# Kernel optimization log

Hardware: AMD Instinct MI355X
Metric: run time of the kernel (lower is better)

## Reference

```python
import jax, jax.numpy as jnp
import numpy as np

H = 48  # hidden_size


def _lstm_cell(inp, h, c, Wih, Whh, bih, bhh):
    # PyTorch LSTMCell: gates ordered (i, f, g, o)
    gates = inp @ Wih.T + h @ Whh.T + bih + bhh
    i, f, g, o = jnp.split(gates, 4, axis=-1)
    i = jax.nn.sigmoid(i)
    f = jax.nn.sigmoid(f)
    g = jnp.tanh(g)
    o = jax.nn.sigmoid(o)
    c_new = f * c + i * g
    h_new = o * jnp.tanh(c_new)
    return h_new, c_new


def setup_inputs() -> dict:
    key = jax.random.key(0)
    ks = jax.random.split(key, 8)
    B, T = 4096, 512
    s = 0.1
    return {
        "x": jax.random.normal(ks[0], (B, T), dtype=jnp.float32),
        "W_ih0": jax.random.normal(ks[1], (4 * H, 1), dtype=jnp.float32) * s,
        "W_hh0": jax.random.normal(ks[2], (4 * H, H), dtype=jnp.float32) * s,
        "b_ih0": jnp.full((4 * H,), 0.01, dtype=jnp.float32),
        "b_hh0": jnp.full((4 * H,), 0.01, dtype=jnp.float32),
        "W_ih1": jax.random.normal(ks[3], (4 * H, H), dtype=jnp.float32) * s,
        "W_hh1": jax.random.normal(ks[4], (4 * H, H), dtype=jnp.float32) * s,
        "b_ih1": jnp.full((4 * H,), 0.01, dtype=jnp.float32),
        "b_hh1": jnp.full((4 * H,), 0.01, dtype=jnp.float32),
        "W_lin": jax.random.normal(ks[5], (1, H), dtype=jnp.float32) * s,
        "b_lin": jnp.full((1,), 0.01, dtype=jnp.float32),
        "future_pred": 64,
    }


def reference(x, W_ih0, W_hh0, b_ih0, b_hh0, W_ih1, W_hh1, b_ih1, b_hh1,
              W_lin, b_lin, future_pred):
    B = x.shape[0]
    h0 = jnp.zeros((B, H), dtype=jnp.float32)
    c0 = jnp.zeros((B, H), dtype=jnp.float32)
    h1 = jnp.zeros((B, H), dtype=jnp.float32)
    c1 = jnp.zeros((B, H), dtype=jnp.float32)

    def tick(h0, c0, h1, c1, inp):  # inp: [B,1]
        h0, c0 = _lstm_cell(inp, h0, c0, W_ih0, W_hh0, b_ih0, b_hh0)
        h1, c1 = _lstm_cell(h0, h1, c1, W_ih1, W_hh1, b_ih1, b_hh1)
        out = h1 @ W_lin.T + b_lin  # [B,1]
        return h0, c0, h1, c1, out

    # teacher-forced pass over observed sequence
    def step_obs(carry, xt):
        h0, c0, h1, c1 = carry
        h0, c0, h1, c1, out = tick(h0, c0, h1, c1, xt)
        return (h0, c0, h1, c1), out

    xs = jnp.swapaxes(x, 0, 1)[:, :, None]  # [T, B, 1]
    (h0, c0, h1, c1), outs_obs = jax.lax.scan(step_obs, (h0, c0, h1, c1), xs)
    last_out = outs_obs[-1]

    def step_fut(carry, _):
        h0, c0, h1, c1, out = carry
        h0, c0, h1, c1, out = tick(h0, c0, h1, c1, out)
        return (h0, c0, h1, c1, out), out

    _, outs_fut = jax.lax.scan(step_fut, (h0, c0, h1, c1, last_out), None,
                               length=future_pred)

    outs = jnp.concatenate([outs_obs, outs_fut], axis=0)  # [T+F, B, 1]
    return jnp.swapaxes(outs[:, :, 0], 0, 1)  # [B, T+F]
```

## Files before the change

kernel.cpp:

```cpp
#include <hip/hip_runtime.h>

#define T_OBS 512
#define RSTRH 264
#define PSTR  28
#define L2E   1.44269504089f

typedef float    f32x4 __attribute__((ext_vector_type(4)));
typedef _Float16 f16x8 __attribute__((ext_vector_type(8)));

#define MF(A,B,C) __builtin_amdgcn_mfma_f32_16x16x32_f16(A,B,C,0,0,0)

__device__ __forceinline__ unsigned f2h(float f){
    union { _Float16 h; unsigned short u; } v; v.h=(_Float16)f; return (unsigned)v.u;
}

__device__ __forceinline__ void bar_lds(){
    asm volatile("s_waitcnt lgkmcnt(0)" ::: "memory");
    __builtin_amdgcn_sched_barrier(0);
    __builtin_amdgcn_s_barrier();
    __builtin_amdgcn_sched_barrier(0);
}

__device__ __forceinline__ float act1(const f32x4 a, float& c){
    const float Ei=__builtin_amdgcn_exp2f(a[0]), Ef=__builtin_amdgcn_exp2f(a[1]);
    const float Eg=__builtin_amdgcn_exp2f(a[2]), Eo=__builtin_amdgcn_exp2f(a[3]);
    const float ui=1.f+Ei, uf=1.f+Ef, ug=1.f+Eg, uo=1.f+Eo;
    const float P=ui*uf, Q=ug*uo;
    const float R=__builtin_amdgcn_rcpf(P*Q);
    const float aP=R*Q, aQ=R*P;
    const float ig=aP*uf, fg=aP*ui;
    const float og=aQ*ug;
    const float gg=fmaf(aQ*uo,-2.f,1.f);
    c = fg*c + ig*gg;
    const float Ec=__builtin_amdgcn_exp2f(2.f*L2E*c);
    return og*fmaf(__builtin_amdgcn_rcpf(1.f+Ec),-2.f,1.f);
}

__device__ __forceinline__ int u_of_pos(const int p){
    return 8*(p>>3) + 4*(p&1) + ((p&7)>>1);
}

__global__ __launch_bounds__(768, 1) void lstm2_v10(
    const float* __restrict__ x,
    const float* __restrict__ Wih0, const float* __restrict__ Whh0,
    const float* __restrict__ bih0, const float* __restrict__ bhh0,
    const float* __restrict__ Wih1, const float* __restrict__ Whh1,
    const float* __restrict__ bih1, const float* __restrict__ bhh1,
    const float* __restrict__ Wlin, const float* __restrict__ blin,
    const int* __restrict__ fut,
    float* __restrict__ out)
{
    __shared__ __attribute__((aligned(16))) _Float16 s_h[16 * RSTRH];
    __shared__ __attribute__((aligned(16))) float s_pr[2][16 * PSTR];
    unsigned* const s32 = (unsigned*)s_h;

    const int tid  = threadIdx.x;
    const int wave = tid >> 6, lane = tid & 63;
    const int q    = lane & 15, rg = lane >> 4;
    const bool isL1 = (wave >= 6);
    const int  w    = isL1 ? wave - 6 : wave;

    for (int i = tid; i < 16 * RSTRH; i += 768) s_h[i] = (_Float16)0.f;

    const float sgl = ((q & 3) == 2) ? 2.f * L2E : -L2E;

    f16x8 ah[2][3], al[2][3];
    #pragma unroll
    for (int i = 0; i < 2; ++i) {
        const int t  = 2 * w + i;
        const int rp = 16 * t + q;
        const int r0 = (rp & 3) * 48 + (rp >> 2);
        #pragma unroll
        for (int s = 0; s < 3; ++s)
            #pragma unroll
            for (int j = 0; j < 8; ++j) {
                const int p = 32 * s + 8 * rg + j;
                float v = 0.f;
                if (isL1) v = ((p < 48) ? Wih1[r0 * 48 + u_of_pos(p)]
                                        : Whh1[r0 * 48 + u_of_pos(p - 48)]) * sgl;
                else if (p < 48) v = Whh0[r0 * 48 + u_of_pos(p)] * sgl;
                const _Float16 hi = (_Float16)v;
                ah[i][s][j] = hi;
                al[i][s][j] = (_Float16)(v - (float)hi);
            }
    }

    const float sg4[4] = { -L2E, -L2E, 2.f * L2E, -L2E };
    f32x4 bvt[2], wi0v[2];
    float wlq[2];
    #pragma unroll
    for (int i = 0; i < 2; ++i) {
        const int u = 8 * w + 4 * i + rg;
        wlq[i] = Wlin[u];
        #pragma unroll
        for (int g = 0; g < 4; ++g) {
            bvt[i][g]  = (isL1 ? (bih1[g*48+u] + bhh1[g*48+u])
                               : (bih0[g*48+u] + bhh0[g*48+u])) * sg4[g];
            wi0v[i][g] = Wih0[g * 48 + u] * sg4[g];
        }
    }

    int koff[3];
    #pragma unroll
    for (int s = 0; s < 3; ++s) {
        const int p0 = 32 * s + 8 * rg;
        koff[s] = p0 + ((p0 >= 48) ? 80 : 0);
    }

    const int F    = fut[0];
    const int TT   = T_OBS + F;
    const int bb0  = blockIdx.x * 16;
    const float bl = blin[0];
    const int xrow = (bb0 + q) * T_OBS;
    const int nbh  = q * RSTRH;
    const int hwp  = nbh + (isL1 ? 128 : 0) + 8 * w + 2 * rg;
    const int prw  = q * PSTR + 4 * w + rg;

    float cc0 = 0.f, cc1 = 0.f;
    const f32x4 z4 = { 0.f, 0.f, 0.f, 0.f };

    __syncthreads();

    if (!isL1) {
        const float x0 = x[xrow];
        const f32x4 a0 = bvt[0] + wi0v[0] * x0;
        const f32x4 a1 = bvt[1] + wi0v[1] * x0;
        const unsigned h0 = f2h(act1(a0, cc0));
        const unsigned h1 = f2h(act1(a1, cc1));
        s32[hwp >> 1] = h0 | (h1 << 16);
    }
    bar_lds();
    float xcur = isL1 ? 0.f : x[xrow + 1];

#define STEADY(TAU_, CB_, PB_) do {                                              \
    if (!isL1) {                                                                 \
        const float xnxt = x[xrow + (((TAU_) + 1 < T_OBS) ? (TAU_) + 1 : T_OBS - 1)]; \
        if ((TAU_) >= 2 && wave == 0) {           \
            const int nn = lane >> 2, j0 = lane & 3;                             \
            const float* pr = &s_pr[((TAU_) - 1) & 1][nn * PSTR];                \
            float sg = pr[j0] + pr[j0+4] + pr[j0+8] + pr[j0+12]                  \
                     + pr[j0+16] + pr[j0+20];                                    \
            sg += __shfl_xor(sg, 1); sg += __shfl_xor(sg, 2);                    \
            if (j0 == 0) out[(bb0 + nn) * TT + ((TAU_) - 2)] = sg + bl;          \
        }                                                                        \
        const f16x8 B0 = *(const f16x8*)(s_h + nbh + (PB_) + koff[0]);           \
        const f16x8 B1 = *(const f16x8*)(s_h + nbh + (PB_) + koff[1]);           \
        f32x4 Aq[2], Bq[2];                                                      \
        _Pragma("unroll")                                                        \
        for (int i = 0; i < 2; ++i) {                                            \
            Aq[i] = MF(ah[i][0], B0, bvt[i]);                                    \
            Aq[i] = MF(al[i][0], B0, Aq[i]);                                     \
            Bq[i] = MF(ah[i][1], B1, z4);                                        \
            Bq[i] = MF(al[i][1], B1, Bq[i]);                                     \
        }                                                                        \
        const f32x4 a0 = Aq[0] + Bq[0] + wi0v[0] * xcur;                         \
        const f32x4 a1 = Aq[1] + Bq[1] + wi0v[1] * xcur;                         \
        const unsigned h0 = f2h(act1(a0, cc0));                                  \
        const unsigned h1 = f2h(act1(a1, cc1));                                  \
        s32[(hwp + (CB_)) >> 1] = h0 | (h1 << 16);                               \
        xcur = xnxt;                                                             \
    } else {                                                                     \
        const f16x8 B0 = *(const f16x8*)(s_h + nbh + (PB_) + koff[0]);           \
        const f16x8 B1 = *(const f16x8*)(s_h + nbh + (PB_) + koff[1]);           \
        const f16x8 B2 = *(const f16x8*)(s_h + nbh + (PB_) + koff[2]);           \
        f32x4 Aq[2], Bq[2];                                                      \
        _Pragma("unroll")                                                        \
        for (int i = 0; i < 2; ++i) {                                            \
            Aq[i] = MF(ah[i][0], B0, bvt[i]);                                    \
            Aq[i] = MF(al[i][0], B0, Aq[i]);                                     \
            Aq[i] = MF(ah[i][1], B1, Aq[i]);                                     \
            Bq[i] = MF(al[i][1], B1, z4);                                        \
            Bq[i] = MF(ah[i][2], B2, Bq[i]);                                     \
            Bq[i] = MF(al[i][2], B2, Bq[i]);                                     \
        }                                                                        \
        const f32x4 a0 = Aq[0] + Bq[0];                                          \
        const f32x4 a1 = Aq[1] + Bq[1];                                          \
        const float h0 = act1(a0, cc0);                                          \
        const float h1 = act1(a1, cc1);                                          \
        s32[(hwp + (CB_)) >> 1] = f2h(h0) | (f2h(h1) << 16);                     \
        s_pr[(TAU_) & 1][prw] = fmaf(h1, wlq[1], h0 * wlq[0]);                   \
    }                                                                            \
    bar_lds();                                                                   \
} while (0)

    for (int tau = 1; tau < T_OBS - 1; tau += 2) {
        STEADY(tau,     64, 0);
        STEADY(tau + 1,  0, 64);
    }
    STEADY(T_OBS - 1, 64, 0);

    if (tid < 16) {
        const float* pr = &s_pr[1][tid * PSTR];
        const f32x4 sv = *(const f32x4*)(pr)      + *(const f32x4*)(pr + 4)
                       + *(const f32x4*)(pr + 8)  + *(const f32x4*)(pr + 12)
                       + *(const f32x4*)(pr + 16) + *(const f32x4*)(pr + 20);
        out[(bb0 + tid) * TT + (T_OBS - 2)] = sv[0] + sv[1] + sv[2] + sv[3] + bl;
    }

    for (int tau = T_OBS; tau <= TT; ++tau) {
        const int cb = (tau & 1) * 64;
        const int pb = cb ^ 64;

        f32x4 Aq[2], Bq[2];
        if (isL1) {
            const f16x8 B0 = *(const f16x8*)(s_h + nbh + pb + koff[0]);
            const f16x8 B1 = *(const f16x8*)(s_h + nbh + pb + koff[1]);
            const f16x8 B2 = *(const f16x8*)(s_h + nbh + pb + koff[2]);
            #pragma unroll
            for (int i = 0; i < 2; ++i) {
                Aq[i] = MF(ah[i][0], B0, bvt[i]);
                Aq[i] = MF(al[i][0], B0, Aq[i]);
                Aq[i] = MF(ah[i][1], B1, Aq[i]);
                Bq[i] = MF(al[i][1], B1, z4);
                Bq[i] = MF(ah[i][2], B2, Bq[i]);
                Bq[i] = MF(al[i][2], B2, Bq[i]);
            }
            const f32x4 a0 = Aq[0] + Bq[0];
            const f32x4 a1 = Aq[1] + Bq[1];
            const float h0 = act1(a0, cc0);
            const float h1 = act1(a1, cc1);
            s32[(hwp + cb) >> 1] = f2h(h0) | (f2h(h1) << 16);
            s_pr[tau & 1][prw] = fmaf(h1, wlq[1], h0 * wlq[0]);
        } else {
            const f16x8 B0 = *(const f16x8*)(s_h + nbh + pb + koff[0]);
            const f16x8 B1 = *(const f16x8*)(s_h + nbh + pb + koff[1]);
            #pragma unroll
            for (int i = 0; i < 2; ++i) {
                Aq[i] = MF(ah[i][0], B0, bvt[i]);
                Aq[i] = MF(al[i][0], B0, Aq[i]);
                Bq[i] = MF(ah[i][1], B1, z4);
                Bq[i] = MF(al[i][1], B1, Bq[i]);
            }
        }
        bar_lds();

        if (!isL1) {
            const float* pr = &s_pr[tau & 1][q * PSTR];
            const f32x4 sv = *(const f32x4*)(pr)      + *(const f32x4*)(pr + 4)
                           + *(const f32x4*)(pr + 8)  + *(const f32x4*)(pr + 12)
                           + *(const f32x4*)(pr + 16) + *(const f32x4*)(pr + 20);
            const float o = sv[0] + sv[1] + sv[2] + sv[3] + bl;
            if (tid < 16) out[(bb0 + q) * TT + (tau - 1)] = o;
            if (tau < TT) {
                const f32x4 a0 = Aq[0] + Bq[0] + wi0v[0] * o;
                const f32x4 a1 = Aq[1] + Bq[1] + wi0v[1] * o;
                const unsigned h0 = f2h(act1(a0, cc0));
                const unsigned h1 = f2h(act1(a1, cc1));
                s32[(hwp + cb) >> 1] = h0 | (h1 << 16);
            }
        }
        bar_lds();
    }
}

extern "C" void kernel_launch(void* const* d_in, const int* in_sizes, int n_in,
                              void* d_out, int out_size, void* d_ws, size_t ws_size,
                              hipStream_t stream) {
    const float* x    = (const float*)d_in[0];
    const float* Wih0 = (const float*)d_in[1];
    const float* Whh0 = (const float*)d_in[2];
    const float* bih0 = (const float*)d_in[3];
    const float* bhh0 = (const float*)d_in[4];
    const float* Wih1 = (const float*)d_in[5];
    const float* Whh1 = (const float*)d_in[6];
    const float* bih1 = (const float*)d_in[7];
    const float* bhh1 = (const float*)d_in[8];
    const float* Wlin = (const float*)d_in[9];
    const float* blin = (const float*)d_in[10];
    const int*   fut  = (const int*)d_in[11];
    float* out = (float*)d_out;

    const int B    = in_sizes[0] / T_OBS;
    const int grid = B / 16;
    lstm2_v10<<<grid, 768, 0, stream>>>(
        x, Wih0, Whh0, bih0, bhh0, Wih1, Whh1, bih1, bhh1, Wlin, blin, fut, out);
}
```

Before: 511.4 us.

## Give every wave both LSTM layers instead of splitting layers across waves

Replaces the split where waves 0-5 ran layer 0 and waves 6-11 ran layer 1, each wave owning two hidden-unit tiles. Now each of the 12 waves owns one tile and computes both layers from a shared interleaved h0/h1 LDS vector, using three f16 MFMA k-blocks for each layer. The per-unit output projection is reduced with lane shuffles before being written to LDS, which shrinks the partial-sum buffer. This balances work across waves and simplifies the LDS layout, but every wave now runs both activation chains serially, and layer 0 wastes MFMA work on zero-padded odd k slots.

```diff
diff --git a/kernel.cpp b/kernel.cpp
--- a/kernel.cpp
+++ b/kernel.cpp
@@ -1,8 +1,8 @@
 #include <hip/hip_runtime.h>
 
 #define T_OBS 512
-#define RSTRH 264
-#define PSTR  28
+#define RDW   100
+#define PSTR  20
 #define L2E   1.44269504089f
 
 typedef float    f32x4 __attribute__((ext_vector_type(4)));
@@ -36,11 +36,7 @@
     return og*fmaf(__builtin_amdgcn_rcpf(1.f+Ec),-2.f,1.f);
 }
 
-__device__ __forceinline__ int u_of_pos(const int p){
-    return 8*(p>>3) + 4*(p&1) + ((p&7)>>1);
-}
-
-__global__ __launch_bounds__(768, 1) void lstm2_v10(
+__global__ __launch_bounds__(768, 1) void lstm2_v12(
     const float* __restrict__ x,
     const float* __restrict__ Wih0, const float* __restrict__ Whh0,
     const float* __restrict__ bih0, const float* __restrict__ bhh0,
@@ -50,204 +46,164 @@
     const int* __restrict__ fut,
     float* __restrict__ out)
 {
-    __shared__ __attribute__((aligned(16))) _Float16 s_h[16 * RSTRH];
+    __shared__ __attribute__((aligned(16))) _Float16 s_h[16 * 2 * RDW];
     __shared__ __attribute__((aligned(16))) float s_pr[2][16 * PSTR];
     unsigned* const s32 = (unsigned*)s_h;
 
     const int tid  = threadIdx.x;
-    const int wave = tid >> 6, lane = tid & 63;
+    const int w    = tid >> 6, lane = tid & 63;
     const int q    = lane & 15, rg = lane >> 4;
-    const bool isL1 = (wave >= 6);
-    const int  w    = isL1 ? wave - 6 : wave;
-
-    for (int i = tid; i < 16 * RSTRH; i += 768) s_h[i] = (_Float16)0.f;
+
+    for (int i = tid; i < 16 * 2 * RDW; i += 768) s32[i % (16*RDW)] = 0u;
 
     const float sgl = ((q & 3) == 2) ? 2.f * L2E : -L2E;
 
-    f16x8 ah[2][3], al[2][3];
-    #pragma unroll
-    for (int i = 0; i < 2; ++i) {
-        const int t  = 2 * w + i;
-        const int rp = 16 * t + q;
+    f16x8 a0h[3], a0l[3], a1h[3], a1l[3];
+    {
+        const int rp = 16 * w + q;
         const int r0 = (rp & 3) * 48 + (rp >> 2);
         #pragma unroll
         for (int s = 0; s < 3; ++s)
             #pragma unroll
             for (int j = 0; j < 8; ++j) {
-                const int p = 32 * s + 8 * rg + j;
-                float v = 0.f;
-                if (isL1) v = ((p < 48) ? Wih1[r0 * 48 + u_of_pos(p)]
-                                        : Whh1[r0 * 48 + u_of_pos(p - 48)]) * sgl;
-                else if (p < 48) v = Whh0[r0 * 48 + u_of_pos(p)] * sgl;
-                const _Float16 hi = (_Float16)v;
-                ah[i][s][j] = hi;
-                al[i][s][j] = (_Float16)(v - (float)hi);
+                const int k = 32 * s + 8 * rg + j;
+                const int u = k >> 1;
+                const int od = k & 1;
+                const float v1 = (od ? Whh1[r0 * 48 + u] : Wih1[r0 * 48 + u]) * sgl;
+                const float v0 = od ? 0.f : Whh0[r0 * 48 + u] * sgl;
+                const _Float16 h1w = (_Float16)v1;
+                const _Float16 h0w = (_Float16)v0;
+                a1h[s][j] = h1w;  a1l[s][j] = (_Float16)(v1 - (float)h1w);
+                a0h[s][j] = h0w;  a0l[s][j] = (_Float16)(v0 - (float)h0w);
             }
     }
 
     const float sg4[4] = { -L2E, -L2E, 2.f * L2E, -L2E };
-    f32x4 bvt[2], wi0v[2];
-    float wlq[2];
+    const int u = 4 * w + rg;
+    f32x4 bv0, bv1, wi0v;
     #pragma unroll
-    for (int i = 0; i < 2; ++i) {
-        const int u = 8 * w + 4 * i + rg;
-        wlq[i] = Wlin[u];
-        #pragma unroll
-        for (int g = 0; g < 4; ++g) {
-            bvt[i][g]  = (isL1 ? (bih1[g*48+u] + bhh1[g*48+u])
-                               : (bih0[g*48+u] + bhh0[g*48+u])) * sg4[g];
-            wi0v[i][g] = Wih0[g * 48 + u] * sg4[g];
-        }
-    }
-
-    int koff[3];
-    #pragma unroll
-    for (int s = 0; s < 3; ++s) {
-        const int p0 = 32 * s + 8 * rg;
-        koff[s] = p0 + ((p0 >= 48) ? 80 : 0);
-    }
-
+    for (int g = 0; g < 4; ++g) {
+        bv0[g]  = (bih0[g*48+u] + bhh0[g*48+u]) * sg4[g];
+        bv1[g]  = (bih1[g*48+u] + bhh1[g*48+u]) * sg4[g];
+        wi0v[g] = Wih0[g * 48 + u] * sg4[g];
+    }
+    const float wl = Wlin[u];
+
+    const int ko0 = 8 * rg, ko1 = 32 + 8 * rg, ko2 = 64 + 8 * rg;
     const int F    = fut[0];
     const int TT   = T_OBS + F;
     const int bb0  = blockIdx.x * 16;
     const float bl = blin[0];
     const int xrow = (bb0 + q) * T_OBS;
-    const int nbh  = q * RSTRH;
-    const int hwp  = nbh + (isL1 ? 128 : 0) + 8 * w + 2 * rg;
-    const int prw  = q * PSTR + 4 * w + rg;
+    const int nbh  = q * 2 * RDW;
+    const int nbd  = q * RDW;
+    const int prw  = lane * PSTR;
 
     float cc0 = 0.f, cc1 = 0.f;
     const f32x4 z4 = { 0.f, 0.f, 0.f, 0.f };
 
     __syncthreads();
 
-    if (!isL1) {
+    {
         const float x0 = x[xrow];
-        const f32x4 a0 = bvt[0] + wi0v[0] * x0;
-        const f32x4 a1 = bvt[1] + wi0v[1] * x0;
-        const unsigned h0 = f2h(act1(a0, cc0));
-        const unsigned h1 = f2h(act1(a1, cc1));
-        s32[hwp >> 1] = h0 | (h1 << 16);
+        const f32x4 a = bv0 + wi0v * x0;
+        const float h0f = act1(a, cc0);
+        s32[nbd + u] = f2h(h0f);
     }
     bar_lds();
-    float xcur = isL1 ? 0.f : x[xrow + 1];
-
-#define STEADY(TAU_, CB_, PB_) do {                                              \
-    if (!isL1) {                                                                 \
-        const float xnxt = x[xrow + (((TAU_) + 1 < T_OBS) ? (TAU_) + 1 : T_OBS - 1)]; \
-        if ((TAU_) >= 2 && wave == 0) {           \
-            const int nn = lane >> 2, j0 = lane & 3;                             \
-            const float* pr = &s_pr[((TAU_) - 1) & 1][nn * PSTR];                \
-            float sg = pr[j0] + pr[j0+4] + pr[j0+8] + pr[j0+12]                  \
-                     + pr[j0+16] + pr[j0+20];                                    \
-            sg += __shfl_xor(sg, 1); sg += __shfl_xor(sg, 2);                    \
-            if (j0 == 0) out[(bb0 + nn) * TT + ((TAU_) - 2)] = sg + bl;          \
-        }                                                                        \
-        const f16x8 B0 = *(const f16x8*)(s_h + nbh + (PB_) + koff[0]);           \
-        const f16x8 B1 = *(const f16x8*)(s_h + nbh + (PB_) + koff[1]);           \
-        f32x4 Aq[2], Bq[2];                                                      \
-        _Pragma("unroll")                                                        \
-        for (int i = 0; i < 2; ++i) {                                            \
-            Aq[i] = MF(ah[i][0], B0, bvt[i]);                                    \
-            Aq[i] = MF(al[i][0], B0, Aq[i]);                                     \
-            Bq[i] = MF(ah[i][1], B1, z4);                                        \
-            Bq[i] = MF(al[i][1], B1, Bq[i]);                                     \
-        }                                                                        \
-        const f32x4 a0 = Aq[0] + Bq[0] + wi0v[0] * xcur;                         \
-        const f32x4 a1 = Aq[1] + Bq[1] + wi0v[1] * xcur;                         \
-        const unsigned h0 = f2h(act1(a0, cc0));                                  \
-        const unsigned h1 = f2h(act1(a1, cc1));                                  \
-        s32[(hwp + (CB_)) >> 1] = h0 | (h1 << 16);                               \
-        xcur = xnxt;                                                             \
-    } else {                                                                     \
-        const f16x8 B0 = *(const f16x8*)(s_h + nbh + (PB_) + koff[0]);           \
-        const f16x8 B1 = *(const f16x8*)(s_h + nbh + (PB_) + koff[1]);           \
-        const f16x8 B2 = *(const f16x8*)(s_h + nbh + (PB_) + koff[2]);           \
-        f32x4 Aq[2], Bq[2];                                                      \
-        _Pragma("unroll")                                                        \
-        for (int i = 0; i < 2; ++i) {                                            \
-            Aq[i] = MF(ah[i][0], B0, bvt[i]);                                    \
-            Aq[i] = MF(al[i][0], B0, Aq[i]);                                     \
-            Aq[i] = MF(ah[i][1], B1, Aq[i]);                                     \
-            Bq[i] = MF(al[i][1], B1, z4);                                        \
-            Bq[i] = MF(ah[i][2], B2, Bq[i]);                                     \
-            Bq[i] = MF(al[i][2], B2, Bq[i]);                                     \
-        }                                                                        \
-        const f32x4 a0 = Aq[0] + Bq[0];                                          \
-        const f32x4 a1 = Aq[1] + Bq[1];                                          \
-        const float h0 = act1(a0, cc0);                                          \
-        const float h1 = act1(a1, cc1);                                          \
-        s32[(hwp + (CB_)) >> 1] = f2h(h0) | (f2h(h1) << 16);                     \
-        s_pr[(TAU_) & 1][prw] = fmaf(h1, wlq[1], h0 * wlq[0]);                   \
+    float xcur = x[xrow + 1];
+
+#define STEADY(TAU_, WB_, RB_) do {                                              \
+    const f16x8 B0 = *(const f16x8*)(s_h + nbh + (RB_) + ko0);                   \
+    const f16x8 B1 = *(const f16x8*)(s_h + nbh + (RB_) + ko1);                   \
+    const f16x8 B2 = *(const f16x8*)(s_h + nbh + (RB_) + ko2);                   \
+    const float xnxt = x[xrow + (((TAU_) + 1 < T_OBS) ? (TAU_) + 1 : T_OBS - 1)]; \
+    f32x4 g1a = MF(a1h[0], B0, bv1);                                             \
+    g1a = MF(a1l[0], B0, g1a);                                                   \
+    g1a = MF(a1h[1], B1, g1a);                                                   \
+    f32x4 g1b = MF(a1l[1], B1, z4);                                              \
+    g1b = MF(a1h[2], B2, g1b);                                                   \
+    g1b = MF(a1l[2], B2, g1b);                                                   \
+    f32x4 g0a = MF(a0h[0], B0, bv0);                                             \
+    g0a = MF(a0l[0], B0, g0a);                                                   \
+    g0a = MF(a0h[1], B1, g0a);                                                   \
+    f32x4 g0b = MF(a0l[1], B1, z4);                                              \
+    g0b = MF(a0h[2], B2, g0b);                                                   \
+    g0b = MF(a0l[2], B2, g0b);                                                   \
+    if ((TAU_) >= 2 && w == 0) {             \
+        const int b = lane >> 2, jj = lane & 3;                                  \
+        const float* pr = &s_pr[((TAU_) - 1) & 1][b * PSTR + jj * 3];            \
+        float gv = pr[0] + pr[1] + pr[2];                                        \
+        gv += __shfl_xor(gv, 1); gv += __shfl_xor(gv, 2);                        \
+        if (jj == 0) out[(bb0 + b) * TT + ((TAU_) - 2)] = gv + bl;               \
     }                                                                            \
+    const f32x4 G1 = g1a + g1b;                                                  \
+    const float h1f = act1(G1, cc1);                                             \
+    const f32x4 G0 = g0a + g0b + wi0v * xcur;                                    \
+    const float h0f = act1(G0, cc0);                                             \
+    s32[nbd + (WB_) + u] = f2h(h0f) | (f2h(h1f) << 16);                          \
+    float part = h1f * wl;                                                       \
+    part += __shfl_xor(part, 16);                                                \
+    part += __shfl_xor(part, 32);                                                \
+    if (lane < 16) s_pr[(TAU_) & 1][prw + w] = part;                             \
+    xcur = xnxt;                                                                 \
     bar_lds();                                                                   \
 } while (0)
 
     for (int tau = 1; tau < T_OBS - 1; tau += 2) {
-        STEADY(tau,     64, 0);
-        STEADY(tau + 1,  0, 64);
-    }
-    STEADY(T_OBS - 1, 64, 0);
+        STEADY(tau,     48, 0);
+        STEADY(tau + 1,  0, 96);
+    }
+    STEADY(T_OBS - 1, 48, 0);
 
     if (tid < 16) {
         const float* pr = &s_pr[1][tid * PSTR];
-        const f32x4 sv = *(const f32x4*)(pr)      + *(const f32x4*)(pr + 4)
-                       + *(const f32x4*)(pr + 8)  + *(const f32x4*)(pr + 12)
-                       + *(const f32x4*)(pr + 16) + *(const f32x4*)(pr + 20);
+        const f32x4 sv = *(const f32x4*)(pr) + *(const f32x4*)(pr + 4)
+                       + *(const f32x4*)(pr + 8);
         out[(bb0 + tid) * TT + (T_OBS - 2)] = sv[0] + sv[1] + sv[2] + sv[3] + bl;
     }
 
     for (int tau = T_OBS; tau <= TT; ++tau) {
-        const int cb = (tau & 1) * 64;
-        const int pb = cb ^ 64;
-
-        f32x4 Aq[2], Bq[2];
-        if (isL1) {
-            const f16x8 B0 = *(const f16x8*)(s_h + nbh + pb + koff[0]);
-            const f16x8 B1 = *(const f16x8*)(s_h + nbh + pb + koff[1]);
-            const f16x8 B2 = *(const f16x8*)(s_h + nbh + pb + koff[2]);
-            #pragma unroll
-            for (int i = 0; i < 2; ++i) {
-                Aq[i] = MF(ah[i][0], B0, bvt[i]);
-                Aq[i] = MF(al[i][0], B0, Aq[i]);
-                Aq[i] = MF(ah[i][1], B1, Aq[i]);
-                Bq[i] = MF(al[i][1], B1, z4);
-                Bq[i] = MF(ah[i][2], B2, Bq[i]);
-                Bq[i] = MF(al[i][2], B2, Bq[i]);
-            }
-            const f32x4 a0 = Aq[0] + Bq[0];
-            const f32x4 a1 = Aq[1] + Bq[1];
-            const float h0 = act1(a0, cc0);
-            const float h1 = act1(a1, cc1);
-            s32[(hwp + cb) >> 1] = f2h(h0) | (f2h(h1) << 16);
-            s_pr[tau & 1][prw] = fmaf(h1, wlq[1], h0 * wlq[0]);
-        } else {
-            const f16x8 B0 = *(const f16x8*)(s_h + nbh + pb + koff[0]);
-            const f16x8 B1 = *(const f16x8*)(s_h + nbh + pb + koff[1]);
-            #pragma unroll
-            for (int i = 0; i < 2; ++i) {
-                Aq[i] = MF(ah[i][0], B0, bvt[i]);
-                Aq[i] = MF(al[i][0], B0, Aq[i]);
-                Bq[i] = MF(ah[i][1], B1, z4);
-                Bq[i] = MF(al[i][1], B1, Bq[i]);
-            }
-        }
+        const int wbh = (tau & 1) * 96;
+        const int rbh = 96 - wbh;
+
+        const f16x8 B0 = *(const f16x8*)(s_h + nbh + rbh + ko0);
+        const f16x8 B1 = *(const f16x8*)(s_h + nbh + rbh + ko1);
+        const f16x8 B2 = *(const f16x8*)(s_h + nbh + rbh + ko2);
+
+        f32x4 g1a = MF(a1h[0], B0, bv1);
+        g1a = MF(a1l[0], B0, g1a);
+        g1a = MF(a1h[1], B1, g1a);
+        f32x4 g1b = MF(a1l[1], B1, z4);
+        g1b = MF(a1h[2], B2, g1b);
+        g1b = MF(a1l[2], B2, g1b);
+        const f32x4 G1 = g1a + g1b;
+        const float h1f = act1(G1, cc1);
+        s_h[nbh + wbh + 2 * u + 1] = (_Float16)h1f;
+        float part = h1f * wl;
+        part += __shfl_xor(part, 16);
+        part += __shfl_xor(part, 32);
+        if (lane < 16) s_pr[tau & 1][prw + w] = part;
+
+        f32x4 g0a = MF(a0h[0], B0, bv0);
+        g0a = MF(a0l[0], B0, g0a);
+        g0a = MF(a0h[1], B1, g0a);
+        f32x4 g0b = MF(a0l[1], B1, z4);
+        g0b = MF(a0h[2], B2, g0b);
+        g0b = MF(a0l[2], B2, g0b);
+        const f32x4 G0p = g0a + g0b;
+
         bar_lds();
 
-        if (!isL1) {
-            const float* pr = &s_pr[tau & 1][q * PSTR];
-            const f32x4 sv = *(const f32x4*)(pr)      + *(const f32x4*)(pr + 4)
-                           + *(const f32x4*)(pr + 8)  + *(const f32x4*)(pr + 12)
-                           + *(const f32x4*)(pr + 16) + *(const f32x4*)(pr + 20);
-            const float o = sv[0] + sv[1] + sv[2] + sv[3] + bl;
-            if (tid < 16) out[(bb0 + q) * TT + (tau - 1)] = o;
-            if (tau < TT) {
-                const f32x4 a0 = Aq[0] + Bq[0] + wi0v[0] * o;
-                const f32x4 a1 = Aq[1] + Bq[1] + wi0v[1] * o;
-                const unsigned h0 = f2h(act1(a0, cc0));
-                const unsigned h1 = f2h(act1(a1, cc1));
-                s32[(hwp + cb) >> 1] = h0 | (h1 << 16);
-            }
+        const float* pr = &s_pr[tau & 1][q * PSTR];
+        const f32x4 sv = *(const f32x4*)(pr) + *(const f32x4*)(pr + 4)
+                       + *(const f32x4*)(pr + 8);
+        const float o = sv[0] + sv[1] + sv[2] + sv[3] + bl;
+        if (tid < 16) out[(bb0 + q) * TT + (tau - 1)] = o;
+        if (tau < TT) {
+            const f32x4 G0 = G0p + wi0v * o;
+            const float h0f = act1(G0, cc0);
+            s_h[nbh + wbh + 2 * u] = (_Float16)h0f;
         }
         bar_lds();
     }
@@ -272,6 +228,6 @@
 
     const int B    = in_sizes[0] / T_OBS;
     const int grid = B / 16;
-    lstm2_v10<<<grid, 768, 0, stream>>>(
+    lstm2_v12<<<grid, 768, 0, stream>>>(
         x, Wih0, Whh0, bih0, bhh0, Wih1, Whh1, bih1, bhh1, Wlin, blin, fut, out);
 }
```

Result: no change. 519.2 us (+1.5%).
